# Performance work log

Measured on AMD Instinct MI355X. Metric: run time of the kernel, lower is better.

Reference implementation:

```python
import jax, jax.numpy as jnp
import numpy as np

B, T = 64, 2048
HID, FAST, SLOW, VOCAB = 256, 64, 256, 64
WRITE_THRESH = 0.4
NEG = -1000000000.0


def setup_inputs() -> dict:
    key = jax.random.key(0)
    ks = jax.random.split(key, 10)
    s = 0.05  # small init so gate sigmoids are not saturated
    return {
        "seq": jax.random.randint(ks[0], (B, T), 0, VOCAB),
        "emb": jax.random.normal(ks[1], (VOCAB, HID), jnp.float32),        # encoder embedding table
        "Wg": jax.random.normal(ks[2], (HID, 1), jnp.float32) * s,         # write_gate
        "bg": jnp.zeros((1,), jnp.float32),
        "Wd": jax.random.normal(ks[3], (HID, 1), jnp.float32) * s,         # demotion_net
        "bd": jnp.zeros((1,), jnp.float32),
        "Wq": jax.random.normal(ks[4], (HID, HID), jnp.float32) * s,       # read_head.q_proj
        "bq": jnp.zeros((HID,), jnp.float32),
        "Wo": jax.random.normal(ks[5], (HID, VOCAB), jnp.float32) * s,     # read_head.out
        "bo": jnp.zeros((VOCAB,), jnp.float32),
    }


def _process_sequence(h, Wg, bg, Wd, bd):
    # h: (B, T, H). Sequential LRU tiered-memory scatter, vectorized over batch.
    Bb, Tt, H = h.shape

    def step(state, tok_h):
        fm, sm, fa, sa, fu, su = state
        ws = jax.nn.sigmoid(tok_h @ Wg + bg)[:, 0]          # (B,) write score
        act = ws >= WRITE_THRESH                            # skip rows with score < 0.4
        fa = fa + fu.astype(jnp.int32)                      # age occupied slots
        sa = sa + su.astype(jnp.int32)
        free = ~fu
        has_free = jnp.any(free, axis=1)                    # (B,)
        free_idx = jnp.argmax(free, axis=1)                 # first free fast slot
        dem = ((fm @ Wd)[..., 0] + bd[0])                   # (B, FAST) demotion scores
        dem_slot = jnp.argmin(dem, axis=1)
        fslot = jnp.where(has_free, free_idx, dem_slot)     # fast slot to write
        foh = jax.nn.one_hot(fslot, FAST, dtype=bool)
        wf = act[:, None] & foh                              # (B, FAST) fast-write mask
        # value demoted to slow (only used when fast was full)
        demoted = jnp.take_along_axis(fm, fslot[:, None, None], axis=1)[:, 0, :]
        slow_act = act & ~has_free
        sfree = ~su
        s_has_free = jnp.any(sfree, axis=1)
        ss = jnp.where(s_has_free, jnp.argmax(sfree, axis=1), jnp.argmax(sa, axis=1))
        soh = jax.nn.one_hot(ss, SLOW, dtype=bool)
        wsm = slow_act[:, None] & soh                        # (B, SLOW) slow-write mask
        sm = jnp.where(wsm[..., None], demoted[:, None, :], sm)
        sa = jnp.where(wsm, 0, sa)
        su = su | wsm
        tok = jax.lax.stop_gradient(tok_h)                   # original writes tok_h.detach()
        fm = jnp.where(wf[..., None], tok[:, None, :], fm)
        fa = jnp.where(wf, 0, fa)
        fu = fu | wf
        return (fm, sm, fa, sa, fu, su), None

    init = (
        jnp.zeros((Bb, FAST, H), h.dtype),
        jnp.zeros((Bb, SLOW, H), h.dtype),
        jnp.zeros((Bb, FAST), jnp.int32),
        jnp.zeros((Bb, SLOW), jnp.int32),
        jnp.zeros((Bb, FAST), bool),
        jnp.zeros((Bb, SLOW), bool),
    )
    hs = jnp.swapaxes(h[:, : Tt - 3], 0, 1)                  # loop runs for T-3 tokens
    (fm, sm, fa, sa, fu, su), _ = jax.lax.scan(step, init, hs)
    memory = jnp.concatenate([fm, sm], axis=1)               # (B, F+S, H)
    mask = jnp.concatenate([fu, su], axis=1).astype(h.dtype)
    slow_mask = su.astype(h.dtype)
    return memory, mask, slow_mask


def reference(seq, emb, Wg, bg, Wd, bd, Wq, bq, Wo, bo):
    h = emb[seq]                                             # encoder: (B, T, H)
    memory, mask, slow_mask = _process_sequence(h, Wg, bg, Wd, bd)
    # ReadHead
    q = h[:, -1, :] @ Wq + bq                                # (B, H)
    scores = jnp.einsum("bnh,bh->bn", memory, q)
    scores = jnp.where(mask == 0, NEG, scores)
    attn = jax.nn.softmax(scores, axis=-1)
    ctx = jnp.einsum("bn,bnh->bh", attn, memory)
    logits = ctx @ Wo + bo                                   # (B, VOCAB)
    return logits, slow_mask
```

## Files before the change

kernel.cpp:

```cpp
#include <hip/hip_runtime.h>
#include <math.h>

#define BB 64
#define TT 2048
#define HIDD 256
#define FASTN 64
#define SLOWN 256
#define VOC 64
#define TLOOP (TT - 3)
#define NEGC -1000000000.0f
#define EPAD 257
#define NEGBIG (-(1 << 20))
#define NW 16
#define NT (NW * 64)


__device__ __forceinline__ int countx(const unsigned char* zs, int lo, int hi,
                                      unsigned LL8) {
  int cnt = 0;
  for (int d = lo & ~3; d < hi; d += 4) {
    unsigned U = *(const unsigned*)(zs + d);
    unsigned m = (LL8 - U) & 0x80808080u;
    if (d < lo) m &= 0x80808080u << ((lo - d) << 3);
    if (d + 4 > hi) m &= 0x80808080u >> ((d + 4 - hi) << 3);
    cnt += __popc(m);
  }
  return cnt;
}

__global__ __launch_bounds__(NT) void k_one(
    const int* __restrict__ seq, const float* __restrict__ emb,
    const float* __restrict__ Wg, const float* __restrict__ bg,
    const float* __restrict__ Wd, const float* __restrict__ bd,
    const float* __restrict__ Wq, const float* __restrict__ bq,
    const float* __restrict__ Wo, const float* __restrict__ bo,
    float* __restrict__ out) {
  const int b = blockIdx.x;
  const int tid = threadIdx.x;
  const int lane = tid & 63;
  const int wv = tid >> 6;

  __shared__ float embS[VOC * EPAD];
  __shared__ __align__(16) unsigned char zsB[2080];
  __shared__ float qLastS[HIDD], ctxS[HIDD];
  __shared__ float pp16[NW][64];
  __shared__ float gp16[NW][64], dp16[NW][64];
  __shared__ float qp4[4][HIDD];
  __shared__ float demS[64], wS[64];
  __shared__ int prS[64], invS[64], cntTok[64];
  __shared__ int CS[NW];
  __shared__ int PsS[NW][64], QsS[NW][64], eSS[NW][64];

  const int2 sq = ((const int2*)(seq + b * TT))[tid];
  const int lastv = seq[b * TT + TT - 1];
  const float4* emb4 = (const float4*)emb;
  for (int i = tid; i < VOC * 64; i += NT) {
    float4 e = emb4[i];
    float* d = &embS[(i >> 6) * EPAD + ((i & 63) << 2)];
    d[0] = e.x; d[1] = e.y; d[2] = e.z; d[3] = e.w;
  }
  __syncthreads();

  {
    const int v = tid & 63, kp = tid >> 6;
    const float* er = &embS[v * EPAD + kp * 16];
    const float* wg = &Wg[kp * 16];
    const float* wd = &Wd[kp * 16];
    float g = 0.f, d = 0.f;
#pragma unroll
    for (int k = 0; k < 16; ++k) { float e = er[k]; g += e * wg[k]; d += e * wd[k]; }
    gp16[kp][v] = g; dp16[kp][v] = d;
  }
  __syncthreads();
  if (tid < 64) {
    float g = bg[0], d = bd[0];
#pragma unroll
    for (int p = 0; p < NW; ++p) { g += gp16[p][tid]; d += dp16[p][tid]; }
    int act = (1.f / (1.f + expf(-g)) >= 0.4f) ? 1 : 0;
    demS[tid] = d;
    float dv = d;
    int r = 0;
    for (int u2 = 0; u2 < 64; ++u2) {
      float du = demS[u2];
      r += (du < dv || (du == dv && u2 < tid)) ? 1 : 0;
    }
    invS[r] = tid;
    prS[tid] = act ? r : 0xFF;
  }
  __syncthreads();

  const int t0 = tid * 2;
  int by0, by1, c;
  {
    int r0 = prS[sq.x], r1 = prS[sq.y];
    by0 = (t0 < TLOOP) ? r0 : 0xFF;
    by1 = (t0 + 1 < TLOOP) ? r1 : 0xFF;
    c = ((by0 != 0xFF) ? 1 : 0) + ((by1 != 0xFF) ? 1 : 0);
  }
  int incl = c;
  for (int s = 1; s < 64; s <<= 1) {
    int t = __shfl_up(incl, s);
    if (lane >= s) incl += t;
  }
  if (lane == 63) CS[wv] = incl;
  __syncthreads();

  int Ow = 0, A = 0;
#pragma unroll
  for (int w2 = 0; w2 < NW; ++w2) {
    int cw = CS[w2];
    Ow += (w2 < wv) ? cw : 0;
    A += cw;
  }
  {
    int pos = Ow + incl - c;
    if (by0 != 0xFF) zsB[pos++] = (unsigned char)by0;
    if (by1 != 0xFF) zsB[pos++] = (unsigned char)by1;
  }
  if (tid < 16) zsB[A + tid] = 0;
  __syncthreads();

  const int fsplit = A < 64 ? A : 64;
  const int nL = A - fsplit;
  const int win = nL < 256 ? nL : 256;
  const int wstart = A - win;
  const int L = (((A + NW - 1) / NW) + 15) & ~15;
  const int baseW = wv * L;
  const int endW = min(baseW + L, A);

  if (tid < 256)
    out[BB * VOC + b * SLOWN + tid] = (tid < win) ? 1.0f : 0.0f;

  const int jq = tid & 255, kq = tid >> 8, kb = kq * 64;
  float wqA[32];
#pragma unroll
  for (int k = 0; k < 32; ++k) wqA[k] = Wq[(kb + k) * HIDD + jq];

  const unsigned LL8 = (unsigned)lane * 0x01010101u | 0x80808080u;
  const int fmin = min(endW, fsplit);
  const int lf = max(baseW, fsplit);
  const int wbl = max(lf, min(endW, wstart));
  int cF = 0, cPre = 0, cWin = 0;
  if (fmin > baseW) cF = countx(zsB, baseW, fmin, LL8);
  if (wbl > lf) cPre = countx(zsB, lf, wbl, LL8);
  if (endW > wbl) cWin = countx(zsB, wbl, endW, LL8);
  const int lenL = endW - lf;
  {
    int P = cF + cPre + cWin - (lenL > 0 ? lenL : 0);
    int Q = (lenL > 0) ? ((zsB[endW - 1] <= lane) ? 1 : 0) : NEGBIG;
    PsS[wv][lane] = P;
    QsS[wv][lane] = Q;
  }
  __syncthreads();

  float qacc = 0.f;
  {
    const float* eL = &embS[lastv * EPAD + kb];
#pragma unroll
    for (int k = 0; k < 32; ++k) qacc += eL[k] * wqA[k];
  }
  float wqB[32];
#pragma unroll
  for (int k = 0; k < 32; ++k) wqB[k] = Wq[(kb + 32 + k) * HIDD + jq];

  int e = 0;
  if (endW > wbl) {
    int a = 0;
    for (int w2 = 0; w2 < wv; ++w2)
      a = max(a + PsS[w2][lane], QsS[w2][lane]);
    a += cF;
    const int lenP = wbl - lf;
    if (lenP > 0) {
      int xl = (zsB[wbl - 1] <= lane) ? 1 : 0;
      a = max(a + cPre - lenP, xl);
    }
    const int n = endW - wbl;
    const int xw = (zsB[endW - 1] <= lane) ? 1 : 0;
    const int Zp = (n - cWin) - (1 - xw);
    const int F = max(0, Zp - a + 1);
    e = n - F;
  }
  eSS[wv][lane] = e;

  {
    const float* eL = &embS[lastv * EPAD + kb + 32];
#pragma unroll
    for (int k = 0; k < 32; ++k) qacc += eL[k] * wqB[k];
  }
  qp4[kq][jq] = qacc;
  __syncthreads();

  if (tid < 64) {
    int af = 0;
#pragma unroll
    for (int w2 = 0; w2 < NW; ++w2)
      af = max(af + PsS[w2][lane], QsS[w2][lane]);
    int et = 0;
#pragma unroll
    for (int w2 = 0; w2 < NW; ++w2) et += eSS[w2][lane];
    int ap = __shfl_up(af, 1); if (lane == 0) ap = 0;
    int ep = __shfl_up(et, 1); if (lane == 0) ep = 0;
    cntTok[invS[lane]] = (af - ap) + (et - ep);
  }
  if (tid < 256)
    qLastS[tid] = qp4[0][tid] + qp4[1][tid] + qp4[2][tid] + qp4[3][tid] + bq[tid];
  __syncthreads();

  const int o = tid & 63, part = tid >> 6;
  float wor[16];
#pragma unroll
  for (int k = 0; k < 16; ++k) wor[k] = Wo[((part << 4) + k) * VOC + o];

  {
    const float* er = &embS[o * EPAD + part * 16];
    const float* qr = &qLastS[part * 16];
    float s = 0.f;
#pragma unroll
    for (int k = 0; k < 16; ++k) s += er[k] * qr[k];
    pp16[part][o] = s;
  }
  __syncthreads();
  if (tid < 64) {
    float sc = 0.f;
#pragma unroll
    for (int p = 0; p < NW; ++p) sc += pp16[p][tid];
    int cc = cntTok[tid];
    float m = (cc > 0) ? sc : NEGC;
    for (int off = 32; off; off >>= 1) m = fmaxf(m, __shfl_xor(m, off));
    float w = (cc > 0) ? (float)cc * expf(sc - m) : 0.f;
    float z = w;
    for (int off = 32; off; off >>= 1) z += __shfl_xor(z, off);
    z += (float)(FASTN + SLOWN - (fsplit + win)) * expf(NEGC - m);
    wS[tid] = w / z;
  }
  __syncthreads();

  if (tid < 256) {
    float cacc = 0.f;
#pragma unroll 16
    for (int u = 0; u < 64; ++u) cacc += wS[u] * embS[u * EPAD + tid];
    ctxS[tid] = cacc;
  }
  __syncthreads();

  {
    const float* cr = &ctxS[part * 16];
    float s = 0.f;
#pragma unroll
    for (int k = 0; k < 16; ++k) s += cr[k] * wor[k];
    pp16[part][o] = s;
  }
  __syncthreads();
  if (tid < 64) {
    float s = bo[tid];
#pragma unroll
    for (int p = 0; p < NW; ++p) s += pp16[p][tid];
    out[b * VOC + tid] = s;
  }
}

extern "C" void kernel_launch(void* const* d_in, const int* in_sizes, int n_in,
                              void* d_out, int out_size, void* d_ws, size_t ws_size,
                              hipStream_t stream) {
  const int*   seq = (const int*)d_in[0];
  const float* emb = (const float*)d_in[1];
  const float* Wg  = (const float*)d_in[2];
  const float* bg  = (const float*)d_in[3];
  const float* Wd  = (const float*)d_in[4];
  const float* bd  = (const float*)d_in[5];
  const float* Wq  = (const float*)d_in[6];
  const float* bq  = (const float*)d_in[7];
  const float* Wo  = (const float*)d_in[8];
  const float* bo  = (const float*)d_in[9];
  float* out = (float*)d_out;

  k_one<<<dim3(64), dim3(NT), 0, stream>>>(seq, emb, Wg, bg, Wd, bd,
                                           Wq, bq, Wo, bo, out);
}
```

Baseline: 85.46 us.

## Fuse gate/demotion dot products into embedding load and parallelize rank via wave shuffles

```diff
diff --git a/kernel.cpp b/kernel.cpp
--- a/kernel.cpp
+++ b/kernel.cpp
@@ -13,6 +13,7 @@
 #define NEGBIG (-(1 << 20))
 #define NW 16
 #define NT (NW * 64)
+#define ACTTH (-0.4054651081081644f)
 
 
 __device__ __forceinline__ int countx(const unsigned char* zs, int lo, int hi,
@@ -44,7 +45,6 @@
   __shared__ __align__(16) unsigned char zsB[2080];
   __shared__ float qLastS[HIDD], ctxS[HIDD];
   __shared__ float pp16[NW][64];
-  __shared__ float gp16[NW][64], dp16[NW][64];
   __shared__ float qp4[4][HIDD];
   __shared__ float demS[64], wS[64];
   __shared__ int prS[64], invS[64], cntTok[64];
@@ -53,39 +53,60 @@
 
   const int2 sq = ((const int2*)(seq + b * TT))[tid];
   const int lastv = seq[b * TT + TT - 1];
+  const int jq = tid & 255, kq = tid >> 8, kb = kq * 64;
+  float wqA[32];
+#pragma unroll
+  for (int k = 0; k < 32; ++k) wqA[k] = Wq[(kb + k) * HIDD + jq];
+
+  const float4 Wg4 = ((const float4*)Wg)[lane];
+  const float4 Wd4 = ((const float4*)Wd)[lane];
+  const float bgv = bg[0];
+
+  float gc[4] = {0.f, 0.f, 0.f, 0.f}, dc[4] = {0.f, 0.f, 0.f, 0.f};
   const float4* emb4 = (const float4*)emb;
-  for (int i = tid; i < VOC * 64; i += NT) {
-    float4 e = emb4[i];
-    float* d = &embS[(i >> 6) * EPAD + ((i & 63) << 2)];
-    d[0] = e.x; d[1] = e.y; d[2] = e.z; d[3] = e.w;
-  }
-  __syncthreads();
-
-  {
-    const int v = tid & 63, kp = tid >> 6;
-    const float* er = &embS[v * EPAD + kp * 16];
-    const float* wg = &Wg[kp * 16];
-    const float* wd = &Wd[kp * 16];
-    float g = 0.f, d = 0.f;
-#pragma unroll
-    for (int k = 0; k < 16; ++k) { float e = er[k]; g += e * wg[k]; d += e * wd[k]; }
-    gp16[kp][v] = g; dp16[kp][v] = d;
-  }
-  __syncthreads();
-  if (tid < 64) {
-    float g = bg[0], d = bd[0];
-#pragma unroll
-    for (int p = 0; p < NW; ++p) { g += gp16[p][tid]; d += dp16[p][tid]; }
-    int act = (1.f / (1.f + expf(-g)) >= 0.4f) ? 1 : 0;
-    demS[tid] = d;
-    float dv = d;
-    int r = 0;
-    for (int u2 = 0; u2 < 64; ++u2) {
-      float du = demS[u2];
-      r += (du < dv || (du == dv && u2 < tid)) ? 1 : 0;
-    }
-    invS[r] = tid;
-    prS[tid] = act ? r : 0xFF;
+#pragma unroll
+  for (int c2 = 0; c2 < 4; ++c2) {
+    float4 e = emb4[c2 * 1024 + tid];
+    float* dst = &embS[(wv + 16 * c2) * EPAD + (lane << 2)];
+    dst[0] = e.x; dst[1] = e.y; dst[2] = e.z; dst[3] = e.w;
+    gc[c2] += e.x * Wg4.x + e.y * Wg4.y + e.z * Wg4.z + e.w * Wg4.w;
+    dc[c2] += e.x * Wd4.x + e.y * Wd4.y + e.z * Wd4.z + e.w * Wd4.w;
+  }
+#pragma unroll
+  for (int off = 1; off < 64; off <<= 1) {
+#pragma unroll
+    for (int c2 = 0; c2 < 4; ++c2) {
+      gc[c2] += __shfl_xor(gc[c2], off);
+      dc[c2] += __shfl_xor(dc[c2], off);
+    }
+  }
+  if (lane < 4) {
+    float dv = lane == 0 ? dc[0] : lane == 1 ? dc[1] : lane == 2 ? dc[2] : dc[3];
+    demS[wv + 16 * lane] = dv;
+  }
+  __syncthreads();
+
+  {
+    float du = demS[lane];
+    int rc[4];
+#pragma unroll
+    for (int c2 = 0; c2 < 4; ++c2) {
+      int v = wv + 16 * c2;
+      rc[c2] = (du < dc[c2] || (du == dc[c2] && lane < v)) ? 1 : 0;
+    }
+#pragma unroll
+    for (int off = 1; off < 64; off <<= 1) {
+#pragma unroll
+      for (int c2 = 0; c2 < 4; ++c2) rc[c2] += __shfl_xor(rc[c2], off);
+    }
+    if (lane < 4) {
+      int rv = lane == 0 ? rc[0] : lane == 1 ? rc[1] : lane == 2 ? rc[2] : rc[3];
+      float gv = lane == 0 ? gc[0] : lane == 1 ? gc[1] : lane == 2 ? gc[2] : gc[3];
+      int v = wv + 16 * lane;
+      int act = (gv + bgv >= ACTTH) ? 1 : 0;
+      prS[v] = act ? rv : 0xFF;
+      invS[rv] = v;
+    }
   }
   __syncthreads();
 
@@ -130,11 +151,6 @@
 
   if (tid < 256)
     out[BB * VOC + b * SLOWN + tid] = (tid < win) ? 1.0f : 0.0f;
-
-  const int jq = tid & 255, kq = tid >> 8, kb = kq * 64;
-  float wqA[32];
-#pragma unroll
-  for (int k = 0; k < 32; ++k) wqA[k] = Wq[(kb + k) * HIDD + jq];
 
   const unsigned LL8 = (unsigned)lane * 0x01010101u | 0x80808080u;
   const int fmin = min(endW, fsplit);
@@ -151,6 +167,9 @@
     PsS[wv][lane] = P;
     QsS[wv][lane] = Q;
   }
+  float wqB[32];
+#pragma unroll
+  for (int k = 0; k < 32; ++k) wqB[k] = Wq[(kb + 32 + k) * HIDD + jq];
   __syncthreads();
 
   float qacc = 0.f;
@@ -159,9 +178,6 @@
 #pragma unroll
     for (int k = 0; k < 32; ++k) qacc += eL[k] * wqA[k];
   }
-  float wqB[32];
-#pragma unroll
-  for (int k = 0; k < 32; ++k) wqB[k] = Wq[(kb + 32 + k) * HIDD + jq];
 
   int e = 0;
   if (endW > wbl) {
@@ -190,7 +206,7 @@
   qp4[kq][jq] = qacc;
   __syncthreads();
 
-  if (tid < 64) {
+  if (wv == 4) {
     int af = 0;
 #pragma unroll
     for (int w2 = 0; w2 < NW; ++w2)
```

New measurement: 84.83 us. About the same (-0.7%).
